# Optimization experiments

Measured on AMD Instinct MI355X. Metric: run time of the kernel, lower is better.

## Reference

```python
import jax, jax.numpy as jnp
import numpy as np

BATCH, OUT_FEATURES = 512, 1024
NUM_BLOCKS, LATTICE_DIM = 32, 4
MAX_INDICES = 256  # q^lattice_dim with q=4, lattice_dim=4


def setup_inputs() -> dict:
    key = jax.random.key(0)
    k1, k2, k3 = jax.random.split(key, 3)
    input_indices = jax.random.randint(k1, (BATCH, NUM_BLOCKS, LATTICE_DIM), 0, MAX_INDICES, dtype=jnp.int64 if jax.config.jax_enable_x64 else jnp.int32)
    weight_indices = jax.random.randint(k2, (OUT_FEATURES, NUM_BLOCKS, LATTICE_DIM), 0, MAX_INDICES, dtype=jnp.int64 if jax.config.jax_enable_x64 else jnp.int32)
    lut_table = jax.random.normal(k3, (MAX_INDICES, MAX_INDICES), dtype=jnp.float32)
    return {"input_indices": input_indices, "weight_indices": weight_indices, "lut_table": lut_table}


def reference(input_indices, weight_indices, lut_table):
    # Flatten block/lattice dims: K = num_blocks * lattice_dim
    B = input_indices.shape[0]
    O = weight_indices.shape[0]
    inp = jnp.clip(input_indices.reshape(B, -1), 0, MAX_INDICES - 1)   # [B, K]
    wgt = jnp.clip(weight_indices.reshape(O, -1), 0, MAX_INDICES - 1)  # [O, K]
    # out[b, o] = sum_k LUT[inp[b, k], wgt[o, k]]
    vals = lut_table[inp[:, None, :], wgt[None, :, :]]  # [B, O, K] gather
    return jnp.sum(vals, axis=-1)  # [B, O]
```

## Files before the change

kernel.cpp:

```cpp
#include <hip/hip_runtime.h>


#define KDIM 128

typedef _Float16 f16x8 __attribute__((ext_vector_type(8)));
typedef float    f32x4 __attribute__((ext_vector_type(4)));

union F16Frag { uint4 u; f16x8 h; };

__global__ __launch_bounds__(1024, 4)
void slt_mfma(const int* __restrict__ inp, const int* __restrict__ wgt,
              const float* __restrict__ lut, float* __restrict__ out)
{
    __shared__ __attribute__((aligned(16))) unsigned char smem[155648];
    unsigned char*  lutB  = smem;
    unsigned short* i_lds = (unsigned short*)(smem + 131072);
    unsigned short* w_lds = (unsigned short*)(smem + 139264);

    const int tid   = threadIdx.x;
    const int otile = blockIdx.x;
    const int btile = blockIdx.y;

    {
        const float4* lut4 = (const float4*)lut;
        #pragma unroll
        for (int it = 0; it < 16; ++it) {
            int idx = it * 1024 + tid;
            float4 v = lut4[idx];
            union { _Float16 h[4]; unsigned long long u; } pk;
            pk.h[0] = (_Float16)v.x; pk.h[1] = (_Float16)v.y;
            pk.h[2] = (_Float16)v.z; pk.h[3] = (_Float16)v.w;
            unsigned r   = (unsigned)idx >> 6;
            unsigned jb  = ((unsigned)idx & 63u) << 3;
            unsigned off = (r << 9) + (jb ^ ((r & 31u) << 4));
            *(unsigned long long*)(lutB + off) = pk.u;
        }
    }

    {
        int b = tid >> 5, kg = tid & 31;
        int4 iv = *(const int4*)(inp + (size_t)(btile * 32 + b) * KDIM + kg * 4);
        i_lds[(kg*4+0)*32 + b] = (unsigned short)(iv.x & 255);
        i_lds[(kg*4+1)*32 + b] = (unsigned short)(iv.y & 255);
        i_lds[(kg*4+2)*32 + b] = (unsigned short)(iv.z & 255);
        i_lds[(kg*4+3)*32 + b] = (unsigned short)(iv.w & 255);
    }
    #pragma unroll
    for (int s2 = 0; s2 < 2; ++s2) {
        int t2 = tid + s2 * 1024;
        int o = t2 >> 5, kg = t2 & 31;
        int4 wv4 = *(const int4*)(wgt + (size_t)(otile * 64 + o) * KDIM + kg * 4);
        w_lds[(kg*4+0)*64 + o] = (unsigned short)(wv4.x & 255);
        w_lds[(kg*4+1)*64 + o] = (unsigned short)(wv4.y & 255);
        w_lds[(kg*4+2)*64 + o] = (unsigned short)(wv4.z & 255);
        w_lds[(kg*4+3)*64 + o] = (unsigned short)(wv4.w & 255);
    }
    __syncthreads();

    const int      lane = tid & 63;
    const int      wid  = tid >> 6;
    const unsigned colq = (unsigned)(lane & 15);
    const unsigned h8   = ((unsigned)((lane >> 4) & 3)) << 3;
    const unsigned h16  = h8 << 1;

    f32x4 zero4 = {0.f, 0.f, 0.f, 0.f};
    f32x4 acc[2][4];
    #pragma unroll
    for (int a = 0; a < 2; ++a)
        #pragma unroll
        for (int b2 = 0; b2 < 4; ++b2)
            acc[a][b2] = zero4;

    #pragma unroll 1
    for (int j = 0; j < 8; ++j) {
        const int ks = wid * 8 + j;

        unsigned i0 = i_lds[ks * 32 + colq];
        unsigned i1 = i_lds[ks * 32 + 16 + colq];
        const unsigned rb0 = i0 << 9, sw0 = (i0 & 31u) << 4;
        const unsigned rb1 = i1 << 9, sw1 = (i1 & 31u) << 4;

        unsigned p[4][4]; unsigned sl[4];
        #pragma unroll
        for (int nt = 0; nt < 4; ++nt) {
            unsigned wv   = w_lds[ks * 64 + nt * 16 + colq];
            unsigned u    = wv - h8;
            unsigned slot = u & 7u;
            unsigned long long pk = 0x3C00ULL << ((slot & 3u) << 4);
            unsigned lo = (unsigned)pk, hi = (unsigned)(pk >> 32);
            unsigned lh    = (slot < 4u);
            unsigned valid = ((u & 31u) < 8u);
            sl[nt] = valid ? (u >> 5) : 0xFFu;
            p[nt][0] = lh ? lo : 0u;
            p[nt][1] = lh ? hi : 0u;
            p[nt][2] = lh ? 0u : lo;
            p[nt][3] = lh ? 0u : hi;
        }

        #pragma unroll
        for (int s = 0; s < 8; ++s) {
            const unsigned su   = (unsigned)s;
            const unsigned offp = su * 64u + h16;
            F16Frag a0, a1;
            a0.u = *(const uint4*)(lutB + rb0 + (offp ^ sw0));
            a1.u = *(const uint4*)(lutB + rb1 + (offp ^ sw1));
            #pragma unroll
            for (int nt = 0; nt < 4; ++nt) {
                F16Frag bb;
                bool take = (sl[nt] == su);
                bb.u.x = take ? p[nt][0] : 0u;
                bb.u.y = take ? p[nt][1] : 0u;
                bb.u.z = take ? p[nt][2] : 0u;
                bb.u.w = take ? p[nt][3] : 0u;
                acc[0][nt] = __builtin_amdgcn_mfma_f32_16x16x32_f16(a0.h, bb.h, acc[0][nt], 0, 0, 0);
                acc[1][nt] = __builtin_amdgcn_mfma_f32_16x16x32_f16(a1.h, bb.h, acc[1][nt], 0, 0, 0);
            }
        }
    }

    __syncthreads();
    f32x4* red = (f32x4*)(smem + 131072);
    #pragma unroll
    for (int t = 0; t < 8; ++t) {
        const int mt = t >> 2, nt = t & 3;
        red[wid * 64 + ((lane >> 4) & 3) * 16 + colq] = acc[mt][nt];
        __syncthreads();
        if (tid < 64) {
            f32x4 sacc = {0.f, 0.f, 0.f, 0.f};
            #pragma unroll
            for (int w = 0; w < 16; ++w) sacc += red[w * 64 + tid];
            const int hh = tid >> 4, cc = tid & 15;
            size_t base = (size_t)(btile * 32 + mt * 16 + hh * 4) * 1024
                        + (size_t)(otile * 64 + nt * 16 + cc);
            out[base]        = sacc[0];
            out[base + 1024] = sacc[1];
            out[base + 2048] = sacc[2];
            out[base + 3072] = sacc[3];
        }
        __syncthreads();
    }
}

extern "C" void kernel_launch(void* const* d_in, const int* in_sizes, int n_in,
                              void* d_out, int out_size, void* d_ws, size_t ws_size,
                              hipStream_t stream) {
    const int*   inp = (const int*)d_in[0];
    const int*   wgt = (const int*)d_in[1];
    const float* lut = (const float*)d_in[2];
    float*       out = (float*)d_out;

    dim3 grid(16, 16);
    dim3 block(1024);
    slt_mfma<<<grid, block, 0, stream>>>(inp, wgt, lut, out);
}
```

Measured before the change: 89.13 us.

## Re-layout LUT in LDS by column slab, split waves over M-tiles, single-pass reduction

Stores the LUT in LDS as eight 16 KB slabs of 64-byte row chunks with a 2-bit XOR swizzle, so each A-fragment load is one base pointer plus a constant slab offset. Work is split so each wave handles one 16-row M-tile over 16 k-steps instead of both M-tiles over 8, and the next row index is prefetched one step ahead. The eight-round reduction with sixteen barriers is replaced by one store of all accumulators, a single barrier, and eight waves each summing one output tile. Per-wave MFMA count stays the same. The trade-offs are a weaker swizzle that may raise LDS bank conflicts and a longer serial k-loop per wave.

After: 97.53 us. +9.4%, slower.

```diff
diff --git a/kernel.cpp b/kernel.cpp
--- a/kernel.cpp
+++ b/kernel.cpp
@@ -30,9 +30,10 @@
             union { _Float16 h[4]; unsigned long long u; } pk;
             pk.h[0] = (_Float16)v.x; pk.h[1] = (_Float16)v.y;
             pk.h[2] = (_Float16)v.z; pk.h[3] = (_Float16)v.w;
-            unsigned r   = (unsigned)idx >> 6;
-            unsigned jb  = ((unsigned)idx & 63u) << 3;
-            unsigned off = (r << 9) + (jb ^ ((r & 31u) << 4));
+            unsigned r  = (unsigned)idx >> 6;
+            unsigned lb = ((unsigned)idx & 63u) << 3;
+            unsigned off = ((lb >> 6) << 14) + (r << 6)
+                         + ((lb & 63u) ^ ((r & 3u) << 4));
             *(unsigned long long*)(lutB + off) = pk.u;
         }
     }
@@ -59,26 +60,25 @@
 
     const int      lane = tid & 63;
     const int      wid  = tid >> 6;
+    const int      mt   = wid & 1;
+    const int      kg   = wid >> 1;
     const unsigned colq = (unsigned)(lane & 15);
     const unsigned h8   = ((unsigned)((lane >> 4) & 3)) << 3;
     const unsigned h16  = h8 << 1;
 
-    f32x4 zero4 = {0.f, 0.f, 0.f, 0.f};
-    f32x4 acc[2][4];
+    f32x4 acc[4];
     #pragma unroll
-    for (int a = 0; a < 2; ++a)
-        #pragma unroll
-        for (int b2 = 0; b2 < 4; ++b2)
-            acc[a][b2] = zero4;
+    for (int nt = 0; nt < 4; ++nt) { f32x4 z = {0.f,0.f,0.f,0.f}; acc[nt] = z; }
+
+    unsigned r_next = i_lds[(kg * 16) * 32 + mt * 16 + colq];
 
     #pragma unroll 1
-    for (int j = 0; j < 8; ++j) {
-        const int ks = wid * 8 + j;
-
-        unsigned i0 = i_lds[ks * 32 + colq];
-        unsigned i1 = i_lds[ks * 32 + 16 + colq];
-        const unsigned rb0 = i0 << 9, sw0 = (i0 & 31u) << 4;
-        const unsigned rb1 = i1 << 9, sw1 = (i1 & 31u) << 4;
+    for (int j = 0; j < 16; ++j) {
+        const int ks = kg * 16 + j;
+        const unsigned r0 = r_next;
+        r_next = i_lds[(((ks + 1) & 127) * 32) + mt * 16 + colq];
+        const unsigned char* pA =
+            lutB + ((r0 << 6) + (h16 ^ ((r0 & 3u) << 4)));
 
         unsigned p[4][4]; unsigned sl[4];
         #pragma unroll
@@ -99,45 +99,40 @@
 
         #pragma unroll
         for (int s = 0; s < 8; ++s) {
-            const unsigned su   = (unsigned)s;
-            const unsigned offp = su * 64u + h16;
-            F16Frag a0, a1;
-            a0.u = *(const uint4*)(lutB + rb0 + (offp ^ sw0));
-            a1.u = *(const uint4*)(lutB + rb1 + (offp ^ sw1));
+            F16Frag a0;
+            a0.u = *(const uint4*)(pA + ((unsigned)s << 14));
             #pragma unroll
             for (int nt = 0; nt < 4; ++nt) {
                 F16Frag bb;
-                bool take = (sl[nt] == su);
+                bool take = (sl[nt] == (unsigned)s);
                 bb.u.x = take ? p[nt][0] : 0u;
                 bb.u.y = take ? p[nt][1] : 0u;
                 bb.u.z = take ? p[nt][2] : 0u;
                 bb.u.w = take ? p[nt][3] : 0u;
-                acc[0][nt] = __builtin_amdgcn_mfma_f32_16x16x32_f16(a0.h, bb.h, acc[0][nt], 0, 0, 0);
-                acc[1][nt] = __builtin_amdgcn_mfma_f32_16x16x32_f16(a1.h, bb.h, acc[1][nt], 0, 0, 0);
+                acc[nt] = __builtin_amdgcn_mfma_f32_16x16x32_f16(a0.h, bb.h, acc[nt], 0, 0, 0);
             }
         }
     }
 
     __syncthreads();
-    f32x4* red = (f32x4*)(smem + 131072);
+    f32x4* red = (f32x4*)smem;
     #pragma unroll
-    for (int t = 0; t < 8; ++t) {
-        const int mt = t >> 2, nt = t & 3;
-        red[wid * 64 + ((lane >> 4) & 3) * 16 + colq] = acc[mt][nt];
-        __syncthreads();
-        if (tid < 64) {
-            f32x4 sacc = {0.f, 0.f, 0.f, 0.f};
-            #pragma unroll
-            for (int w = 0; w < 16; ++w) sacc += red[w * 64 + tid];
-            const int hh = tid >> 4, cc = tid & 15;
-            size_t base = (size_t)(btile * 32 + mt * 16 + hh * 4) * 1024
-                        + (size_t)(otile * 64 + nt * 16 + cc);
-            out[base]        = sacc[0];
-            out[base + 1024] = sacc[1];
-            out[base + 2048] = sacc[2];
-            out[base + 3072] = sacc[3];
-        }
-        __syncthreads();
+    for (int nt = 0; nt < 4; ++nt)
+        red[wid * 256 + nt * 64 + lane] = acc[nt];
+    __syncthreads();
+
+    if (wid < 8) {
+        const int mt2 = wid >> 2;
+        const int nt2 = wid & 3;
+        f32x4 s4 = {0.f, 0.f, 0.f, 0.f};
+        #pragma unroll
+        for (int g = 0; g < 8; ++g)
+            s4 += red[(g * 2 + mt2) * 256 + nt2 * 64 + lane];
+        const int rrow = btile * 32 + mt2 * 16 + ((lane >> 4) & 3) * 4;
+        const int ccol = otile * 64 + nt2 * 16 + (lane & 15);
+        #pragma unroll
+        for (int c = 0; c < 4; ++c)
+            out[(size_t)(rrow + c) * 1024 + ccol] = s4[c];
     }
 }
 
```
